# Optimization experiments

Measured on AMD Instinct MI355X. Metric: run time of the kernel, lower is better.

The kernel has to match this reference:

```python
import jax, jax.numpy as jnp
import numpy as np

B, S, D, H = 8, 1024, 1024, 16
DK = D // H
EPS = 1e-5

def _layernorm(x, w, b):
    mu = jnp.mean(x, axis=-1, keepdims=True)
    var = jnp.mean((x - mu) ** 2, axis=-1, keepdims=True)
    return (x - mu) * jax.lax.rsqrt(var + EPS) * w + b

def setup_inputs() -> dict:
    key = jax.random.key(0)
    ks = jax.random.split(key, 12)
    x = jax.random.normal(ks[0], (B, S, D), dtype=jnp.float32)
    batch_lengths = jax.random.randint(ks[1], (B,), S // 2, S + 1, dtype=jnp.int32)
    sc = 1.0 / np.sqrt(D)
    Wq = jax.random.normal(ks[2], (H, D, DK), dtype=jnp.float32) * sc
    Wk = jax.random.normal(ks[3], (H, D, DK), dtype=jnp.float32) * sc
    Wv = jax.random.normal(ks[4], (H, D, DK), dtype=jnp.float32) * sc
    fc1_w = jax.random.normal(ks[5], (D, D), dtype=jnp.float32) * sc
    fc1_b = jnp.zeros((D,), dtype=jnp.float32)
    fc2_w = jax.random.normal(ks[6], (D, D), dtype=jnp.float32) * sc
    fc2_b = jnp.zeros((D,), dtype=jnp.float32)
    ln1_w = jnp.ones((D,), dtype=jnp.float32)
    ln1_b = jnp.zeros((D,), dtype=jnp.float32)
    ln2_w = jnp.ones((D,), dtype=jnp.float32)
    ln2_b = jnp.zeros((D,), dtype=jnp.float32)
    return {"x": x, "Wq": Wq, "Wk": Wk, "Wv": Wv, "fc1_w": fc1_w, "fc1_b": fc1_b,
            "fc2_w": fc2_w, "fc2_b": fc2_b, "ln1_w": ln1_w, "ln1_b": ln1_b,
            "ln2_w": ln2_w, "ln2_b": ln2_b, "batch_lengths": batch_lengths, "max_len": S}

def reference(x, Wq, Wk, Wv, fc1_w, fc1_b, fc2_w, fc2_b, ln1_w, ln1_b, ln2_w, ln2_b, batch_lengths, max_len):
    b, s, d = x.shape
    h, _, dk = Wq.shape
    # padding masks: valid positions are t < length
    row = (jnp.arange(s)[None, :] < batch_lengths[:, None]).astype(x.dtype)  # [B,S]
    m = row[:, :, None]                 # [B,S,1], outputMask per-row
    mh = m[:, None]                     # [B,1,S,1]
    # all heads batched: Q,K,V -> [B,H,S,dk], masked like Wq(ctx)*mask etc.
    Q = jnp.einsum('bsd,hde->bhse', x, Wq) * mh
    K = jnp.einsum('bsd,hde->bhse', x, Wk) * mh
    V = jnp.einsum('bsd,hde->bhse', x, Wv) * mh
    energy = jnp.einsum('bhqe,bhke->bhqk', Q, K)
    # attnMask: key columns beyond length -> -inf
    key_valid = row[:, None, None, :] > 0
    energy = jnp.where(key_valid, energy, -jnp.inf)
    score = jax.nn.softmax(energy / jnp.sqrt(jnp.asarray(dk, x.dtype)), axis=-1)
    z = jnp.einsum('bhqk,bhke->bhqe', score, V)           # [B,H,S,dk]
    z = z.transpose(0, 2, 1, 3).reshape(b, s, d) * m      # concat heads, mask
    x1 = _layernorm(x + z, ln1_w, ln1_b)
    ff = jax.nn.relu(x1 @ fc1_w + fc1_b) * m
    ff = (ff @ fc2_w + fc2_b) * m
    return _layernorm(x1 + ff, ln2_w, ln2_b)
```

## Files before the change

### kernel.cpp

```cpp
#include <hip/hip_runtime.h>
#include <math.h>

#define B_ 8
#define S_ 1024
#define D_ 1024
#define H_ 16
#define DK_ 64
#define EPS_ 1e-5f

typedef __bf16 bf16_t;
typedef __bf16 bf16x8 __attribute__((ext_vector_type(8)));
typedef __bf16 bf16x4v __attribute__((ext_vector_type(4)));
typedef float  f32x4  __attribute__((ext_vector_type(4)));

__device__ __forceinline__ void gld16(const void* g, void* l) {
    __builtin_amdgcn_global_load_lds(
        (const __attribute__((address_space(1))) void*)g,
        (__attribute__((address_space(3))) void*)l, 16, 0, 0);
}

__global__ __launch_bounds__(256)
void prep(const float* __restrict__ x,
          const float* __restrict__ Wq, const float* __restrict__ Wk,
          const float* __restrict__ Wv, const float* __restrict__ W1,
          const float* __restrict__ W2, bf16_t* __restrict__ xb,
          bf16_t* __restrict__ WtQKV, bf16_t* __restrict__ Wt1,
          bf16_t* __restrict__ Wt2)
{
    __shared__ float tile[64][65];
    const int tid = threadIdx.x;
    const int z = blockIdx.z;

    if (z >= 5) {
        const int blk = (z - 5) * 256 + blockIdx.y * 16 + blockIdx.x;
        const int i = (blk * 256 + tid) * 4;
        const float4 v = *(const float4*)(x + i);
        bf16x4v o = { (bf16_t)v.x, (bf16_t)v.y, (bf16_t)v.z, (bf16_t)v.w };
        *(bf16x4v*)(xb + i) = o;
        return;
    }

    const int n0 = blockIdx.x * 64, k0 = blockIdx.y * 64;
    const int col = tid & 63, r0 = tid >> 6;
    const float* src = (z == 0) ? Wq : (z == 1) ? Wk : (z == 2) ? Wv
                     : (z == 3) ? W1 : W2;
    #pragma unroll
    for (int i = 0; i < 16; i++) {
        const int row = r0 + i * 4;
        float v;
        if (z < 3)
            v = src[((size_t)(n0 >> 6) << 16) + (size_t)(k0 + row) * 64 + col];
        else
            v = src[(size_t)(k0 + row) * D_ + n0 + col];
        tile[row][col] = v;
    }
    __syncthreads();
    bf16_t* dst = (z < 3) ? (WtQKV + (size_t)z * D_ * D_)
                : (z == 3) ? Wt1 : Wt2;
    #pragma unroll
    for (int i = 0; i < 16; i++) {
        const int nr = r0 + i * 4;
        dst[(size_t)(n0 + nr) * D_ + k0 + col] = (bf16_t)tile[col][nr];
    }
}

template<int EPI, typename OUT>
__global__ __launch_bounds__(512, 2)
void gemm8(const bf16_t* __restrict__ A, const bf16_t* __restrict__ Bw,
           const float* __restrict__ bias, const int* __restrict__ lens,
           OUT* __restrict__ C, int M, int N, int K)
{
    __shared__ __align__(16) bf16_t As[2][256 * 64];
    __shared__ __align__(16) bf16_t Bs[2][256 * 64];

    const int tid  = threadIdx.x;
    const int lane = tid & 63;
    const int w    = tid >> 6;
    const int quad = lane >> 4, l16 = lane & 15;
    const int wm = w & 1, wn = w >> 1;
    const int bn = blockIdx.x * 256, bm = blockIdx.y * 256;
    const int sw8 = l16 & 7;

    const int ci0 = tid, ci1 = tid + 512;
    const int aB0 = ci0 >> 9, aR0 = (ci0 >> 3) & 63;
    const int aC0 = (((ci0 & 7) ^ (aR0 & 7)) << 3);
    const int aB1 = ci1 >> 9, aR1 = (ci1 >> 3) & 63;
    const int aC1 = (((ci1 & 7) ^ (aR1 & 7)) << 3);
    const int bB0 = ci0 >> 8, bR0 = (ci0 >> 3) & 31;
    const int bC0 = (((ci0 & 7) ^ (bR0 & 7)) << 3);
    const int bB1 = ci1 >> 8, bR1 = (ci1 >> 3) & 31;
    const int bC1 = (((ci1 & 7) ^ (bR1 & 7)) << 3);
    const int u0 = w * 64, u1 = 512 + w * 64;
    const int adD0 = (u0 >> 9) * 16384 + (u0 & 511) * 16;
    const int adD1 = (u1 >> 9) * 16384 + (u1 & 511) * 16;
    const int bdD0 = (u0 >> 8) * 8192 + (u0 & 255) * 16;
    const int bdD1 = (u1 >> 8) * 8192 + (u1 & 255) * 16;

    f32x4 acc[8][4];
    #pragma unroll
    for (int i = 0; i < 8; i++)
        #pragma unroll
        for (int j = 0; j < 4; j++)
            #pragma unroll
            for (int r = 0; r < 4; r++) acc[i][j][r] = 0.f;

#define STAGE_A(h, nb_, kt_) { \
    char* d_ = (char*)As[nb_] + (h) * 8192; \
    gld16(A + (size_t)(bm + aB0 * 128 + (h) * 64 + aR0) * K + (kt_) * 64 + aC0, d_ + adD0); \
    gld16(A + (size_t)(bm + aB1 * 128 + (h) * 64 + aR1) * K + (kt_) * 64 + aC1, d_ + adD1); }
#define STAGE_B(h, nb_, kt_) { \
    char* d_ = (char*)Bs[nb_] + (h) * 4096; \
    gld16(Bw + (size_t)(bn + bB0 * 64 + (h) * 32 + bR0) * K + (kt_) * 64 + bC0, d_ + bdD0); \
    gld16(Bw + (size_t)(bn + bB1 * 64 + (h) * 32 + bR1) * K + (kt_) * 64 + bC1, d_ + bdD1); }
#define RD_A(dst, base, qm_, i_, kh_) \
    dst = *(const bf16x8*)&base[(wm * 128 + (qm_) * 64 + (i_) * 16 + l16) * 64 + ((((kh_) * 4 + quad) ^ sw8) << 3)];
#define RD_B(dst, base, qn_, j_, kh_) \
    dst = *(const bf16x8*)&base[(wn * 64 + (qn_) * 32 + (j_) * 16 + l16) * 64 + ((((kh_) * 4 + quad) ^ sw8) << 3)];
#define MM(QI, QJ, AF, BF) \
    _Pragma("unroll") \
    for (int kh_ = 0; kh_ < 2; kh_++) \
        _Pragma("unroll") \
        for (int i_ = 0; i_ < 4; i_++) \
            _Pragma("unroll") \
            for (int j_ = 0; j_ < 2; j_++) \
                acc[(QI) * 4 + i_][(QJ) * 2 + j_] = __builtin_amdgcn_mfma_f32_16x16x32_bf16( \
                    AF[i_][kh_], BF[j_][kh_], acc[(QI) * 4 + i_][(QJ) * 2 + j_], 0, 0, 0);
#define MIDBAR() { __builtin_amdgcn_s_barrier(); \
    asm volatile("s_waitcnt lgkmcnt(0)" ::: "memory"); }

    const int NKT = K >> 6;

    STAGE_A(0, 0, 0);
    STAGE_B(0, 0, 0);
    STAGE_B(1, 0, 0);
    STAGE_A(1, 0, 0);
    asm volatile("s_waitcnt vmcnt(4)" ::: "memory");
    __builtin_amdgcn_s_barrier();

    for (int t = 0; t < NKT; ++t) {
        const int cb = t & 1, nb = cb ^ 1;
        const int ktn = (t + 1 < NKT) ? t + 1 : t;
        const bf16_t* Ac = As[cb];
        const bf16_t* Bc = Bs[cb];

        bf16x8 fa[4][2], fb[2][2];
        #pragma unroll
        for (int i = 0; i < 4; i++) { RD_A(fa[i][0], Ac, 0, i, 0); RD_A(fa[i][1], Ac, 0, i, 1); }
        #pragma unroll
        for (int j = 0; j < 2; j++) { RD_B(fb[j][0], Bc, 0, j, 0); RD_B(fb[j][1], Bc, 0, j, 1); }
        STAGE_A(0, nb, ktn);
        MIDBAR();
        __builtin_amdgcn_s_setprio(1);
        MM(0, 0, fa, fb);
        __builtin_amdgcn_s_setprio(0);
        asm volatile("s_waitcnt vmcnt(4)" ::: "memory");
        __builtin_amdgcn_s_barrier();

        bf16x8 gb[2][2];
        #pragma unroll
        for (int j = 0; j < 2; j++) { RD_B(gb[j][0], Bc, 1, j, 0); RD_B(gb[j][1], Bc, 1, j, 1); }
        STAGE_B(0, nb, ktn);
        MIDBAR();
        __builtin_amdgcn_s_setprio(1);
        MM(0, 1, fa, gb);
        __builtin_amdgcn_s_setprio(0);
        asm volatile("s_waitcnt vmcnt(4)" ::: "memory");
        __builtin_amdgcn_s_barrier();

        bf16x8 ga[4][2];
        #pragma unroll
        for (int i = 0; i < 4; i++) { RD_A(ga[i][0], Ac, 1, i, 0); RD_A(ga[i][1], Ac, 1, i, 1); }
        STAGE_B(1, nb, ktn);
        MIDBAR();
        __builtin_amdgcn_s_setprio(1);
        MM(1, 1, ga, gb);
        __builtin_amdgcn_s_setprio(0);
        __builtin_amdgcn_s_barrier();

        STAGE_A(1, nb, ktn);
        MIDBAR();
        __builtin_amdgcn_s_setprio(1);
        MM(1, 0, ga, fb);
        __builtin_amdgcn_s_setprio(0);
        asm volatile("s_waitcnt vmcnt(4)" ::: "memory");
        __builtin_amdgcn_s_barrier();
    }

#undef STAGE_A
#undef STAGE_B
#undef RD_A
#undef RD_B
#undef MM
#undef MIDBAR

    #pragma unroll
    for (int ii = 0; ii < 8; ii++) {
        #pragma unroll
        for (int r = 0; r < 4; r++) {
            const int m = bm + wm * 128 + (ii >> 2) * 64 + (ii & 3) * 16 + quad * 4 + r;
            float keep = 1.f;
            if (EPI != 0) {
                const int s = m & (S_ - 1);
                const int bb = m >> 10;
                keep = (s < lens[bb]) ? 1.f : 0.f;
            }
            #pragma unroll
            for (int jj = 0; jj < 4; jj++) {
                const int n = bn + wn * 64 + (jj >> 1) * 32 + (jj & 1) * 16 + l16;
                float v = acc[ii][jj][r];
                if (EPI != 0) {
                    v += bias[n];
                    if (EPI == 1) v = fmaxf(v, 0.f);
                    v *= keep;
                }
                C[(size_t)m * N + n] = (OUT)v;
            }
        }
    }
}

__global__ __launch_bounds__(256, 3)
void attn_mfma(const bf16_t* __restrict__ QKV, const int* __restrict__ lens,
               bf16_t* __restrict__ Z)
{
    __shared__ __align__(16) bf16_t Ks[2][64][64];
    __shared__ __align__(16) bf16_t Vt[2][64][72];
    __shared__ __align__(16) bf16_t Ps[64][72];

    const int tid  = threadIdx.x;
    const int lane = tid & 63;
    const int w    = tid >> 6;
    const int quad = lane >> 4;
    const int l16  = lane & 15;
    const int id   = blockIdx.x;
    const int b    = id & 7;
    const int h    = (id >> 3) & 15;
    const int qt   = id >> 7;
    const int len  = lens[b];
    const int qbase = qt * 64;
    const bf16_t* Qp = QKV + (size_t)b * S_ * 3072 + (size_t)h * 64;
    const bf16_t* Kp = Qp + 1024;
    const bf16_t* Vp = Qp + 2048;
    const size_t zbase = (size_t)b * S_ * D_ + (size_t)h * 64;

    if (qbase >= len) {
        const int r = tid >> 2, c0 = (tid & 3) * 16;
        bf16_t* zp = Z + zbase + (size_t)(qbase + r) * D_ + c0;
        uint4 zz = {0u, 0u, 0u, 0u};
        *(uint4*)zp = zz;
        *(uint4*)(zp + 8) = zz;
        return;
    }

    const int qrow = qbase + w * 16 + l16;
    const bf16x8 bq0 = *(const bf16x8*)(Qp + (size_t)qrow * 3072 + quad * 8);
    const bf16x8 bq1 = *(const bf16x8*)(Qp + (size_t)qrow * 3072 + 32 + quad * 8);

    const int kr0  = tid >> 3;
    const int kpos = tid & 7;
    const int kc0  = (kpos ^ (kr0 & 7)) << 3;
    const int kc1  = (kpos ^ ((kr0 + 32) & 7)) << 3;

    const int vr  = tid >> 2;
    const int vc0 = (tid & 3) * 16;
    const int vp  = vr ^ ((tid & 3) << 4);

    f32x4 o[4];
    #pragma unroll
    for (int dm = 0; dm < 4; dm++)
        #pragma unroll
        for (int r = 0; r < 4; r++) o[dm][r] = 0.f;
    float l_q = 0.f;

    const int ntiles = (len + 63) >> 6;

    gld16(Kp + (size_t)kr0 * 3072 + kc0,
          (char*)&Ks[0][0][0] + (size_t)(w * 64) * 16);
    gld16(Kp + (size_t)(kr0 + 32) * 3072 + kc1,
          (char*)&Ks[0][0][0] + (size_t)(256 + w * 64) * 16);
    bf16x8 vcur0 = *(const bf16x8*)(Vp + (size_t)vr * 3072 + vc0);
    bf16x8 vcur1 = *(const bf16x8*)(Vp + (size_t)vr * 3072 + vc0 + 8);
    __syncthreads();

    for (int t = 0; t < ntiles; t++) {
        const int k0 = t * 64;
        const int cb = t & 1, nb = (t + 1) & 1;
        const int kn0 = (t + 1 < ntiles ? t + 1 : t) * 64;

        gld16(Kp + (size_t)(kn0 + kr0) * 3072 + kc0,
              (char*)&Ks[nb][0][0] + (size_t)(w * 64) * 16);
        gld16(Kp + (size_t)(kn0 + kr0 + 32) * 3072 + kc1,
              (char*)&Ks[nb][0][0] + (size_t)(256 + w * 64) * 16);
        const bf16_t* vsrc = Vp + (size_t)(kn0 + vr) * 3072 + vc0;
        const bf16x8 vn0 = *(const bf16x8*)vsrc;
        const bf16x8 vn1 = *(const bf16x8*)(vsrc + 8);
        __builtin_amdgcn_sched_barrier(0);

        #pragma unroll
        for (int kt = 0; kt < 4; kt++) {
            const int r = kt * 16 + l16;
            const bf16x8 ak0 = *(const bf16x8*)&Ks[cb][r][(quad ^ (l16 & 7)) << 3];
            const bf16x8 ak1 = *(const bf16x8*)&Ks[cb][r][((4 + quad) ^ (l16 & 7)) << 3];
            f32x4 z4 = {0.f, 0.f, 0.f, 0.f};
            z4 = __builtin_amdgcn_mfma_f32_16x16x32_bf16(ak0, bq0, z4, 0, 0, 0);
            const f32x4 sfv = __builtin_amdgcn_mfma_f32_16x16x32_bf16(ak1, bq1, z4, 0, 0, 0);
            bf16x4v pk;
            #pragma unroll
            for (int r2 = 0; r2 < 4; r2++) {
                const int key = k0 + kt * 16 + quad * 4 + r2;
                float p = __expf(sfv[r2] * 0.125f);
                p = (key < len) ? p : 0.f;
                l_q += p;
                pk[r2] = (bf16_t)p;
            }
            *(bf16x4v*)&Ps[w * 16 + l16][kt * 16 + quad * 4] = pk;
        }

        #pragma unroll
        for (int i = 0; i < 8; i++) Vt[cb][vc0 + i][vp] = vcur0[i];
        #pragma unroll
        for (int i = 0; i < 8; i++) Vt[cb][vc0 + 8 + i][vp] = vcur1[i];
        vcur0 = vn0;
        vcur1 = vn1;
        __syncthreads();

        const bf16x8 bp0 = *(const bf16x8*)&Ps[w * 16 + l16][quad * 8];
        const bf16x8 bp1 = *(const bf16x8*)&Ps[w * 16 + l16][32 + quad * 8];
        #pragma unroll
        for (int dm = 0; dm < 4; dm++) {
            const bf16x8 av0 = *(const bf16x8*)&Vt[cb][dm * 16 + l16][(quad * 8) ^ (dm * 16)];
            const bf16x8 av1 = *(const bf16x8*)&Vt[cb][dm * 16 + l16][(32 + quad * 8) ^ (dm * 16)];
            o[dm] = __builtin_amdgcn_mfma_f32_16x16x32_bf16(av0, bp0, o[dm], 0, 0, 0);
            o[dm] = __builtin_amdgcn_mfma_f32_16x16x32_bf16(av1, bp1, o[dm], 0, 0, 0);
        }
    }

    l_q += __shfl_xor(l_q, 16);
    l_q += __shfl_xor(l_q, 32);
    const int qg = qbase + w * 16 + l16;
    const float inv = (qg < len) ? 1.f / l_q : 0.f;
    bf16_t* zrow = Z + zbase + (size_t)qg * D_;
    #pragma unroll
    for (int dm = 0; dm < 4; dm++) {
        bf16x4v st;
        #pragma unroll
        for (int r = 0; r < 4; r++) st[r] = (bf16_t)(o[dm][r] * inv);
        *(bf16x4v*)(zrow + dm * 16 + quad * 4) = st;
    }
}

__device__ __forceinline__ void ln_core(float vx, float vy, float vz, float vw,
                                        int tid, float& mean, float& rstd)
{
    __shared__ float red[8];
    float s = vx + vy + vz + vw;
    #pragma unroll
    for (int off = 32; off; off >>= 1) s += __shfl_xor(s, off, 64);
    const int wv = tid >> 6, lane = tid & 63;
    if (lane == 0) red[wv] = s;
    __syncthreads();
    mean = (red[0] + red[1] + red[2] + red[3]) * (1.f / D_);
    const float dx = vx - mean, dy = vy - mean, dz = vz - mean, dw = vw - mean;
    float s2 = dx * dx + dy * dy + dz * dz + dw * dw;
    #pragma unroll
    for (int off = 32; off; off >>= 1) s2 += __shfl_xor(s2, off, 64);
    if (lane == 0) red[4 + wv] = s2;
    __syncthreads();
    rstd = rsqrtf((red[4] + red[5] + red[6] + red[7]) * (1.f / D_) + EPS_);
}

__global__ __launch_bounds__(256)
void add_ln1(const float* __restrict__ X, const bf16_t* __restrict__ Y,
             const float* __restrict__ g, const float* __restrict__ beta,
             bf16_t* __restrict__ out)
{
    const int row = blockIdx.x, tid = threadIdx.x;
    const float4 xv = ((const float4*)(X + (size_t)row * D_))[tid];
    const bf16x4v yv = *(const bf16x4v*)(Y + (size_t)row * D_ + tid * 4);
    const float vx = xv.x + (float)yv[0], vy = xv.y + (float)yv[1];
    const float vz = xv.z + (float)yv[2], vw = xv.w + (float)yv[3];
    float mean, rstd;
    ln_core(vx, vy, vz, vw, tid, mean, rstd);
    const float4 gv = ((const float4*)g)[tid];
    const float4 bv = ((const float4*)beta)[tid];
    bf16x4v o;
    o[0] = (bf16_t)((vx - mean) * rstd * gv.x + bv.x);
    o[1] = (bf16_t)((vy - mean) * rstd * gv.y + bv.y);
    o[2] = (bf16_t)((vz - mean) * rstd * gv.z + bv.z);
    o[3] = (bf16_t)((vw - mean) * rstd * gv.w + bv.w);
    *(bf16x4v*)(out + (size_t)row * D_ + tid * 4) = o;
}

__global__ __launch_bounds__(256)
void add_ln2(const bf16_t* __restrict__ X, const float* __restrict__ Y,
             const float* __restrict__ g, const float* __restrict__ beta,
             float* __restrict__ out)
{
    const int row = blockIdx.x, tid = threadIdx.x;
    const bf16x4v xv = *(const bf16x4v*)(X + (size_t)row * D_ + tid * 4);
    const float4 yv = ((const float4*)(Y + (size_t)row * D_))[tid];
    const float vx = (float)xv[0] + yv.x, vy = (float)xv[1] + yv.y;
    const float vz = (float)xv[2] + yv.z, vw = (float)xv[3] + yv.w;
    float mean, rstd;
    ln_core(vx, vy, vz, vw, tid, mean, rstd);
    const float4 gv = ((const float4*)g)[tid];
    const float4 bv = ((const float4*)beta)[tid];
    float4 o;
    o.x = (vx - mean) * rstd * gv.x + bv.x;
    o.y = (vy - mean) * rstd * gv.y + bv.y;
    o.z = (vz - mean) * rstd * gv.z + bv.z;
    o.w = (vw - mean) * rstd * gv.w + bv.w;
    ((float4*)(out + (size_t)row * D_))[tid] = o;
}

extern "C" void kernel_launch(void* const* d_in, const int* in_sizes, int n_in,
                              void* d_out, int out_size, void* d_ws, size_t ws_size,
                              hipStream_t stream)
{
    const float* x    = (const float*)d_in[0];
    const float* Wq   = (const float*)d_in[1];
    const float* Wk   = (const float*)d_in[2];
    const float* Wv   = (const float*)d_in[3];
    const float* fc1w = (const float*)d_in[4];
    const float* fc1b = (const float*)d_in[5];
    const float* fc2w = (const float*)d_in[6];
    const float* fc2b = (const float*)d_in[7];
    const float* ln1w = (const float*)d_in[8];
    const float* ln1b = (const float*)d_in[9];
    const float* ln2w = (const float*)d_in[10];
    const float* ln2b = (const float*)d_in[11];
    const int*   lens = (const int*)d_in[12];
    float* out = (float*)d_out;

    char* ws = (char*)d_ws;
    const size_t MB = 1024 * 1024;
    bf16_t* QKVb  = (bf16_t*)(ws);
    bf16_t* Zb    = (bf16_t*)(ws + 48 * MB);
    bf16_t* X1b   = (bf16_t*)(ws + 80 * MB);
    bf16_t* xb    = (bf16_t*)(ws + 96 * MB);
    bf16_t* H1b   = (bf16_t*)(ws + 96 * MB);
    float*  FF    = (float*)(ws + 48 * MB);
    bf16_t* WtQKV = (bf16_t*)(ws + 112 * MB);
    bf16_t* Wt1   = (bf16_t*)(ws + 118 * MB);
    bf16_t* Wt2   = (bf16_t*)(ws + 120 * MB);

    const int M = B_ * S_;

    prep<<<dim3(16, 16, 37), 256, 0, stream>>>(x, Wq, Wk, Wv, fc1w, fc2w,
                                               xb, WtQKV, Wt1, Wt2);

    gemm8<0, bf16_t><<<dim3(3072 / 256, M / 256), 512, 0, stream>>>(
        xb, WtQKV, nullptr, nullptr, QKVb, M, 3072, D_);

    attn_mfma<<<dim3(2048), 256, 0, stream>>>(QKVb, lens, Zb);

    add_ln1<<<M, 256, 0, stream>>>(x, Zb, ln1w, ln1b, X1b);

    gemm8<1, bf16_t><<<dim3(D_ / 256, M / 256), 512, 0, stream>>>(
        X1b, Wt1, fc1b, lens, H1b, M, D_, D_);
    gemm8<2, float><<<dim3(D_ / 256, M / 256), 512, 0, stream>>>(
        H1b, Wt2, fc2b, lens, FF, M, D_, D_);

    add_ln2<<<M, 256, 0, stream>>>(X1b, FF, ln2w, ln2b, out);
}
```

Before: 347.7 us.

## Restructure GEMM pipeline, add BN template, swizzle block order, narrower FFN tiles

Replaces the four-phase interleaved staging and MIDBAR scheme with one prefetch of the whole next K-tile at the start of each iteration, followed by one barrier and all MFMA work. Adds a BN template parameter so the two FFN GEMMs use 256x128 tiles, which doubles their grid size to fill more CUs. Also adds an XCD-style blockIdx swizzle to improve L2 locality. The coarser double buffering may expose more load latency, and the narrower tiles lower arithmetic intensity per block.

```diff
diff --git a/kernel.cpp b/kernel.cpp
--- a/kernel.cpp
+++ b/kernel.cpp
@@ -64,58 +64,57 @@
     }
 }
 
-template<int EPI, typename OUT>
+template<int EPI, int BN, typename OUT>
 __global__ __launch_bounds__(512, 2)
 void gemm8(const bf16_t* __restrict__ A, const bf16_t* __restrict__ Bw,
            const float* __restrict__ bias, const int* __restrict__ lens,
            OUT* __restrict__ C, int M, int N, int K)
 {
+    constexpr int NSB = BN / 64;
+    constexpr int WN  = BN / 4;
+    constexpr int NJ  = WN / 16;
+
     __shared__ __align__(16) bf16_t As[2][256 * 64];
-    __shared__ __align__(16) bf16_t Bs[2][256 * 64];
+    __shared__ __align__(16) bf16_t Bs[2][BN * 64];
 
     const int tid  = threadIdx.x;
     const int lane = tid & 63;
     const int w    = tid >> 6;
     const int quad = lane >> 4, l16 = lane & 15;
     const int wm = w & 1, wn = w >> 1;
-    const int bn = blockIdx.x * 256, bm = blockIdx.y * 256;
     const int sw8 = l16 & 7;
 
-    const int ci0 = tid, ci1 = tid + 512;
-    const int aB0 = ci0 >> 9, aR0 = (ci0 >> 3) & 63;
-    const int aC0 = (((ci0 & 7) ^ (aR0 & 7)) << 3);
-    const int aB1 = ci1 >> 9, aR1 = (ci1 >> 3) & 63;
-    const int aC1 = (((ci1 & 7) ^ (aR1 & 7)) << 3);
-    const int bB0 = ci0 >> 8, bR0 = (ci0 >> 3) & 31;
-    const int bC0 = (((ci0 & 7) ^ (bR0 & 7)) << 3);
-    const int bB1 = ci1 >> 8, bR1 = (ci1 >> 3) & 31;
-    const int bC1 = (((ci1 & 7) ^ (bR1 & 7)) << 3);
-    const int u0 = w * 64, u1 = 512 + w * 64;
-    const int adD0 = (u0 >> 9) * 16384 + (u0 & 511) * 16;
-    const int adD1 = (u1 >> 9) * 16384 + (u1 & 511) * 16;
-    const int bdD0 = (u0 >> 8) * 8192 + (u0 & 255) * 16;
-    const int bdD1 = (u1 >> 8) * 8192 + (u1 & 255) * 16;
-
-    f32x4 acc[8][4];
+    const int nwg  = gridDim.x * gridDim.y;
+    const int orig = blockIdx.y * gridDim.x + blockIdx.x;
+    const int swz  = (orig & 7) * (nwg >> 3) + (orig >> 3);
+    const int bn = (swz % gridDim.x) * BN;
+    const int bm = (swz / gridDim.x) * 256;
+
+    const int rS  = tid >> 3;
+    const int cS  = ((tid & 7) ^ (rS & 7)) << 3;
+    const int dOf = w * 64 * 16;
+
+    f32x4 acc[8][NJ];
     #pragma unroll
     for (int i = 0; i < 8; i++)
         #pragma unroll
-        for (int j = 0; j < 4; j++)
+        for (int j = 0; j < NJ; j++)
             #pragma unroll
             for (int r = 0; r < 4; r++) acc[i][j][r] = 0.f;
 
-#define STAGE_A(h, nb_, kt_) { \
-    char* d_ = (char*)As[nb_] + (h) * 8192; \
-    gld16(A + (size_t)(bm + aB0 * 128 + (h) * 64 + aR0) * K + (kt_) * 64 + aC0, d_ + adD0); \
-    gld16(A + (size_t)(bm + aB1 * 128 + (h) * 64 + aR1) * K + (kt_) * 64 + aC1, d_ + adD1); }
-#define STAGE_B(h, nb_, kt_) { \
-    char* d_ = (char*)Bs[nb_] + (h) * 4096; \
-    gld16(Bw + (size_t)(bn + bB0 * 64 + (h) * 32 + bR0) * K + (kt_) * 64 + bC0, d_ + bdD0); \
-    gld16(Bw + (size_t)(bn + bB1 * 64 + (h) * 32 + bR1) * K + (kt_) * 64 + bC1, d_ + bdD1); }
-#define RD_A(dst, base, qm_, i_, kh_) \
-    dst = *(const bf16x8*)&base[(wm * 128 + (qm_) * 64 + (i_) * 16 + l16) * 64 + ((((kh_) * 4 + quad) ^ sw8) << 3)];
-#define RD_B(dst, base, qn_, j_, kh_) \
-    dst = *(const bf16x8*)&base[(wn * 64 + (qn_) * 32 + (j_) * 16 + l16) * 64 + ((((kh_) * 4 + quad) ^ sw8) << 3)];
+#define STAGE(buf_, kt_) { \
+    _Pragma("unroll") \
+    for (int s_ = 0; s_ < 4; s_++) \
+        gld16(A + (size_t)(bm + s_ * 64 + rS) * K + (kt_) * 64 + cS, \
+              (char*)As[buf_] + s_ * 8192 + dOf); \
+    _Pragma("unroll") \
+    for (int s_ = 0; s_ < NSB; s_++) \
+        gld16(Bw + (size_t)(bn + s_ * 64 + rS) * K + (kt_) * 64 + cS, \
+              (char*)Bs[buf_] + s_ * 8192 + dOf); }
+#define RD_A(dst, qm_, i_, kh_) \
+    dst = *(const bf16x8*)&Ac[(wm * 128 + (qm_) * 64 + (i_) * 16 + l16) * 64 + ((((kh_) * 4 + quad) ^ sw8) << 3)];
+#define RD_B(dst, qn_, j_, kh_) \
+    dst = *(const bf16x8*)&Bc[(wn * WN + (qn_) * 32 + (j_) * 16 + l16) * 64 + ((((kh_) * 4 + quad) ^ sw8) << 3)];
 #define MM(QI, QJ, AF, BF) \
     _Pragma("unroll") \
     for (int kh_ = 0; kh_ < 2; kh_++) \
@@ -125,17 +124,10 @@
             for (int j_ = 0; j_ < 2; j_++) \
                 acc[(QI) * 4 + i_][(QJ) * 2 + j_] = __builtin_amdgcn_mfma_f32_16x16x32_bf16( \
                     AF[i_][kh_], BF[j_][kh_], acc[(QI) * 4 + i_][(QJ) * 2 + j_], 0, 0, 0);
-#define MIDBAR() { __builtin_amdgcn_s_barrier(); \
-    asm volatile("s_waitcnt lgkmcnt(0)" ::: "memory"); }
 
     const int NKT = K >> 6;
 
-    STAGE_A(0, 0, 0);
-    STAGE_B(0, 0, 0);
-    STAGE_B(1, 0, 0);
-    STAGE_A(1, 0, 0);
-    asm volatile("s_waitcnt vmcnt(4)" ::: "memory");
-    __builtin_amdgcn_s_barrier();
+    STAGE(0, 0);
 
     for (int t = 0; t < NKT; ++t) {
         const int cb = t & 1, nb = cb ^ 1;
@@ -143,55 +135,55 @@
         const bf16_t* Ac = As[cb];
         const bf16_t* Bc = Bs[cb];
 
+        STAGE(nb, ktn);
+        if constexpr (BN == 256)
+            asm volatile("s_waitcnt vmcnt(8)" ::: "memory");
+        else
+            asm volatile("s_waitcnt vmcnt(6)" ::: "memory");
+        __builtin_amdgcn_sched_barrier(0);
+        __builtin_amdgcn_s_barrier();
+        __builtin_amdgcn_sched_barrier(0);
+
         bf16x8 fa[4][2], fb[2][2];
         #pragma unroll
-        for (int i = 0; i < 4; i++) { RD_A(fa[i][0], Ac, 0, i, 0); RD_A(fa[i][1], Ac, 0, i, 1); }
-        #pragma unroll
-        for (int j = 0; j < 2; j++) { RD_B(fb[j][0], Bc, 0, j, 0); RD_B(fb[j][1], Bc, 0, j, 1); }
-        STAGE_A(0, nb, ktn);
-        MIDBAR();
+        for (int i = 0; i < 4; i++) { RD_A(fa[i][0], 0, i, 0); RD_A(fa[i][1], 0, i, 1); }
+        #pragma unroll
+        for (int j = 0; j < 2; j++) { RD_B(fb[j][0], 0, j, 0); RD_B(fb[j][1], 0, j, 1); }
         __builtin_amdgcn_s_setprio(1);
         MM(0, 0, fa, fb);
         __builtin_amdgcn_s_setprio(0);
-        asm volatile("s_waitcnt vmcnt(4)" ::: "memory");
+
+        if constexpr (BN == 256) {
+            bf16x8 gb[2][2];
+            #pragma unroll
+            for (int j = 0; j < 2; j++) { RD_B(gb[j][0], 1, j, 0); RD_B(gb[j][1], 1, j, 1); }
+            __builtin_amdgcn_s_setprio(1);
+            MM(0, 1, fa, gb);
+            __builtin_amdgcn_s_setprio(0);
+            bf16x8 ga[4][2];
+            #pragma unroll
+            for (int i = 0; i < 4; i++) { RD_A(ga[i][0], 1, i, 0); RD_A(ga[i][1], 1, i, 1); }
+            __builtin_amdgcn_s_setprio(1);
+            MM(1, 1, ga, gb);
+            MM(1, 0, ga, fb);
+            __builtin_amdgcn_s_setprio(0);
+        } else {
+            bf16x8 ga[4][2];
+            #pragma unroll
+            for (int i = 0; i < 4; i++) { RD_A(ga[i][0], 1, i, 0); RD_A(ga[i][1], 1, i, 1); }
+            __builtin_amdgcn_s_setprio(1);
+            MM(1, 0, ga, fb);
+            __builtin_amdgcn_s_setprio(0);
+        }
+
+        __builtin_amdgcn_sched_barrier(0);
         __builtin_amdgcn_s_barrier();
-
-        bf16x8 gb[2][2];
-        #pragma unroll
-        for (int j = 0; j < 2; j++) { RD_B(gb[j][0], Bc, 1, j, 0); RD_B(gb[j][1], Bc, 1, j, 1); }
-        STAGE_B(0, nb, ktn);
-        MIDBAR();
-        __builtin_amdgcn_s_setprio(1);
-        MM(0, 1, fa, gb);
-        __builtin_amdgcn_s_setprio(0);
-        asm volatile("s_waitcnt vmcnt(4)" ::: "memory");
-        __builtin_amdgcn_s_barrier();
-
-        bf16x8 ga[4][2];
-        #pragma unroll
-        for (int i = 0; i < 4; i++) { RD_A(ga[i][0], Ac, 1, i, 0); RD_A(ga[i][1], Ac, 1, i, 1); }
-        STAGE_B(1, nb, ktn);
-        MIDBAR();
-        __builtin_amdgcn_s_setprio(1);
-        MM(1, 1, ga, gb);
-        __builtin_amdgcn_s_setprio(0);
-        __builtin_amdgcn_s_barrier();
-
-        STAGE_A(1, nb, ktn);
-        MIDBAR();
-        __builtin_amdgcn_s_setprio(1);
-        MM(1, 0, ga, fb);
-        __builtin_amdgcn_s_setprio(0);
-        asm volatile("s_waitcnt vmcnt(4)" ::: "memory");
-        __builtin_amdgcn_s_barrier();
-    }
-
-#undef STAGE_A
-#undef STAGE_B
+    }
+
+#undef STAGE
 #undef RD_A
 #undef RD_B
 #undef MM
-#undef MIDBAR
 
     #pragma unroll
     for (int ii = 0; ii < 8; ii++) {
@@ -205,8 +197,8 @@
                 keep = (s < lens[bb]) ? 1.f : 0.f;
             }
             #pragma unroll
-            for (int jj = 0; jj < 4; jj++) {
-                const int n = bn + wn * 64 + (jj >> 1) * 32 + (jj & 1) * 16 + l16;
+            for (int jj = 0; jj < NJ; jj++) {
+                const int n = bn + wn * WN + (jj >> 1) * 32 + (jj & 1) * 16 + l16;
                 float v = acc[ii][jj][r];
                 if (EPI != 0) {
                     v += bias[n];
@@ -449,16 +441,16 @@
     prep<<<dim3(16, 16, 37), 256, 0, stream>>>(x, Wq, Wk, Wv, fc1w, fc2w,
                                                xb, WtQKV, Wt1, Wt2);
 
-    gemm8<0, bf16_t><<<dim3(3072 / 256, M / 256), 512, 0, stream>>>(
+    gemm8<0, 256, bf16_t><<<dim3(3072 / 256, M / 256), 512, 0, stream>>>(
         xb, WtQKV, nullptr, nullptr, QKVb, M, 3072, D_);
 
     attn_mfma<<<dim3(2048), 256, 0, stream>>>(QKVb, lens, Zb);
 
     add_ln1<<<M, 256, 0, stream>>>(x, Zb, ln1w, ln1b, X1b);
 
-    gemm8<1, bf16_t><<<dim3(D_ / 256, M / 256), 512, 0, stream>>>(
+    gemm8<1, 128, bf16_t><<<dim3(D_ / 128, M / 256), 512, 0, stream>>>(
         X1b, Wt1, fc1b, lens, H1b, M, D_, D_);
-    gemm8<2, float><<<dim3(D_ / 256, M / 256), 512, 0, stream>>>(
+    gemm8<2, 128, float><<<dim3(D_ / 128, M / 256), 512, 0, stream>>>(
         H1b, Wt2, fc2b, lens, FF, M, D_, D_);
 
     add_ln2<<<M, 256, 0, stream>>>(X1b, FF, ln2w, ln2b, out);
```

New measurement: 330.0 us. -5.1%, faster.
